# Kernel optimization log

Hardware: AMD Instinct MI355X
Metric: run time of the kernel (lower is better)

Reference implementation:

```python
import jax, jax.numpy as jnp
import numpy as np
from jax import lax

B, T_SRC, C_IN = 32, 1024, 512
CH, T_DE = 256, 4096
K, K_EMB = 5, 3
LEAKY = 0.3
EPS = 1e-5


def setup_inputs() -> dict:
    key = jax.random.key(0)
    ks = jax.random.split(key, 8)
    s = 0.02
    return {
        "x": jax.random.normal(ks[0], (B, T_SRC, C_IN), jnp.float32),
        "target": jax.random.normal(ks[1], (B, 1, T_DE), jnp.float32),
        "dr": jax.random.randint(ks[2], (B, T_SRC), 0, 4),
        "mask": jnp.zeros((B, T_SRC), bool),
        "w_conv1": jax.random.normal(ks[3], (CH, C_IN, K), jnp.float32) * s,
        "b_conv1": jnp.zeros((CH,), jnp.float32),
        "ln1_g": jnp.ones((CH,), jnp.float32),
        "ln1_b": jnp.zeros((CH,), jnp.float32),
        "w_conv2": jax.random.normal(ks[4], (CH, CH, K), jnp.float32) * s,
        "b_conv2": jnp.zeros((CH,), jnp.float32),
        "ln2_g": jnp.ones((CH,), jnp.float32),
        "ln2_b": jnp.zeros((CH,), jnp.float32),
        "w_lin": jax.random.normal(ks[5], (CH, 1), jnp.float32) * s,
        "b_lin": jnp.zeros((1,), jnp.float32),
        "w_emb": jax.random.normal(ks[6], (CH, 1, K_EMB), jnp.float32) * s,
        "b_emb": jnp.zeros((CH,), jnp.float32),
    }


def _conv1d(x, w, b, pad):
    # x: [B, C_in, T], w: [C_out, C_in, K]
    y = lax.conv_general_dilated(x, w, (1,), [(pad, pad)], dimension_numbers=("NCH", "OIH", "NCH"))
    return y + b[None, :, None]


def _layernorm(x, g, b):
    m = jnp.mean(x, -1, keepdims=True)
    v = jnp.var(x, -1, keepdims=True)
    return (x - m) * lax.rsqrt(v + EPS) * g + b


def _average_over_durations(values, durs):
    # values: [B, 1, T_de], durs: [B, T_en] -> [B, 1, T_en]
    ends = jnp.cumsum(durs, 1)                                   # [B, T_en]
    starts = jnp.pad(ends[:, :-1], ((0, 0), (1, 0)))
    nz_cum = jnp.pad(jnp.cumsum((values != 0.0).astype(jnp.float32), 2), ((0, 0), (0, 0), (1, 0)))
    v_cum = jnp.pad(jnp.cumsum(values, 2), ((0, 0), (0, 0), (1, 0)))
    dce = ends[:, None, :]
    dcs = starts[:, None, :]
    sums = jnp.take_along_axis(v_cum, dce, 2) - jnp.take_along_axis(v_cum, dcs, 2)
    nel = jnp.take_along_axis(nz_cum, dce, 2) - jnp.take_along_axis(nz_cum, dcs, 2)
    return jnp.where(nel == 0.0, 0.0, sums / nel)


def reference(x, target, dr, mask, w_conv1, b_conv1, ln1_g, ln1_b, w_conv2, b_conv2, ln2_g, ln2_b, w_lin, b_lin, w_emb, b_emb):
    # VariancePredictor: [conv -> leaky_relu -> layernorm] x2 -> linear -> mask (eval mode, dropout off)
    h = _conv1d(x.transpose(0, 2, 1), w_conv1, b_conv1, (K - 1) // 2).transpose(0, 2, 1)
    h = _layernorm(jax.nn.leaky_relu(h, LEAKY), ln1_g, ln1_b)
    h = _conv1d(h.transpose(0, 2, 1), w_conv2, b_conv2, (K - 1) // 2).transpose(0, 2, 1)
    h = _layernorm(jax.nn.leaky_relu(h, LEAKY), ln2_g, ln2_b)
    energy_pred = (h @ w_lin + b_lin)[..., 0]                     # [B, T_src]
    energy_pred = jnp.where(mask, 0.0, energy_pred)
    avg_energy_target = _average_over_durations(target, dr)       # [B, 1, T_src]
    energy_emb = _conv1d(avg_energy_target, w_emb, b_emb, (K_EMB - 1) // 2)  # [B, CH, T_src]
    return energy_pred, avg_energy_target, energy_emb
```

## Files before the change

### kernel.cpp

```cpp
#include <hip/hip_runtime.h>

typedef __attribute__((ext_vector_type(8))) short short8;
typedef __attribute__((ext_vector_type(4))) float f32x4;

#define LEAKY_F 0.3f

typedef __attribute__((address_space(3))) void lds_t;
typedef __attribute__((address_space(1))) void gmem_t;
#define G2L(g, l) __builtin_amdgcn_global_load_lds((const gmem_t*)(g), (lds_t*)(l), 16, 0, 0)

__device__ __forceinline__ unsigned short f2bf(float f) {
    union { float f; unsigned u; } v; v.f = f;
    unsigned u = v.u;
    return (unsigned short)((u + 0x7fffu + ((u >> 16) & 1u)) >> 16);
}
__device__ __forceinline__ float bf2f(unsigned short u) {
    union { unsigned u; float f; } v; v.u = ((unsigned)u) << 16; return v.f;
}

__global__ void cast_pad_x(const float* __restrict__ in, unsigned short* __restrict__ out) {
    int i = blockIdx.x * 256 + threadIdx.x;
    long g = (long)i * 8;
    int row = (int)(g >> 9);
    int b = row >> 10;
    long o = ((long)(row + (b << 2) + 2) << 9) + (g & 511);
    const float4* p = (const float4*)(in + g);
    float4 a = p[0], c = p[1];
    union { unsigned short s[8]; uint4 v; } u;
    u.s[0] = f2bf(a.x); u.s[1] = f2bf(a.y); u.s[2] = f2bf(a.z); u.s[3] = f2bf(a.w);
    u.s[4] = f2bf(c.x); u.s[5] = f2bf(c.y); u.s[6] = f2bf(c.z); u.s[7] = f2bf(c.w);
    *(uint4*)(out + o) = u.v;
}

__global__ void zero_pads(unsigned short* __restrict__ p, int cin) {
    int j = blockIdx.x * 256 + threadIdx.x;
    int upb = cin >> 1;
    int b = j / upb, rem = j % upb;
    int upr = cin >> 3;
    int r4 = rem / upr;
    int col = (rem % upr) * 8;
    int rowp = (r4 < 2) ? r4 : (r4 + 1024);
    *(uint4*)(p + ((long)b * 1028 + rowp) * cin + col) = make_uint4(0u, 0u, 0u, 0u);
}

__global__ void prep_w(const float* __restrict__ w, unsigned short* __restrict__ out, int CIN, int n) {
    int i = blockIdx.x * 256 + threadIdx.x;
    if (i >= n) return;
    int ch = i / (CIN * 5);
    int rem = i % (CIN * 5);
    int tap = rem / CIN;
    int cin = rem % CIN;
    out[ch * (5 * CIN) + tap * CIN + cin] = f2bf(w[(ch * CIN + cin) * 5 + tap]);
}

template<int CIN, bool PRED>
__global__ __launch_bounds__(512, 1) void gemm_conv_fused(
    const unsigned short* __restrict__ A,
    const unsigned short* __restrict__ W,
    const float* __restrict__ bias,
    const float* __restrict__ gam,
    const float* __restrict__ bet,
    const float* __restrict__ wlin,
    const float* __restrict__ blin,
    const unsigned char* __restrict__ mask,
    unsigned short* __restrict__ Yln,
    float* __restrict__ Ypred)
{
    constexpr int KW = 5 * CIN;
    constexpr int S  = KW / 64;
    constexpr int ASLOT = 128 * 64;
    constexpr int BSLOT = 256 * 64;
    __shared__ __align__(16) unsigned short smem[3 * (ASLOT + BSLOT)];

    const int tid = threadIdx.x, lane = tid & 63, wid = tid >> 6;
    const int wm = wid >> 2, wn = wid & 3;
    const int blk = blockIdx.x;
    const int bb = blk >> 3, tl0 = (blk & 7) << 7;
    const long rowbase = (long)bb * 1028 + tl0;

    long asrc[2]; int adst[2];
    #pragma unroll
    for (int c = 0; c < 2; c++) {
        int u = ((c * 8 + wid) << 6) + lane;
        int r = u >> 3, sg = (u & 7) ^ (r & 7);
        asrc[c] = (rowbase + r) * (long)CIN + sg * 8;
        adst[c] = (c * 8 + wid) << 9;
    }
    long bsrc[4]; int bdst[4];
    #pragma unroll
    for (int c = 0; c < 4; c++) {
        int u = ((c * 8 + wid) << 6) + lane;
        int r = u >> 3, sg = (u & 7) ^ (r & 7);
        bsrc[c] = (long)r * KW + sg * 8;
        bdst[c] = (c * 8 + wid) << 9;
    }

    f32x4 acc[4][4] = {};

    auto stage = [&](int t, int slot) {
        const int k0 = t * 64;
        unsigned short* a = smem + slot * ASLOT;
        unsigned short* b = smem + 3 * ASLOT + slot * BSLOT;
        #pragma unroll
        for (int c = 0; c < 2; c++) G2L(A + asrc[c] + k0, a + adst[c]);
        #pragma unroll
        for (int c = 0; c < 4; c++) G2L(W + bsrc[c] + k0, b + bdst[c]);
    };

    const int l15 = lane & 15, lhi = (lane >> 4) & 3;
    const int arow = (wm * 64 + l15) * 64;
    const int brow = (wn * 64 + l15) * 64;
    const int sw = l15 & 7;

    auto compute = [&](int slot) {
        const unsigned short* ab = smem + slot * ASLOT;
        const unsigned short* bp = smem + 3 * ASLOT + slot * BSLOT;
        #pragma unroll
        for (int kh = 0; kh < 2; kh++) {
            short8 af[4], bg[4];
            const int sgoff = (((kh << 2) | lhi) ^ sw) << 3;
            #pragma unroll
            for (int m = 0; m < 4; m++)
                af[m] = *(const short8*)&ab[arow + m * 1024 + sgoff];
            #pragma unroll
            for (int n = 0; n < 4; n++)
                bg[n] = *(const short8*)&bp[brow + n * 1024 + sgoff];
            asm volatile("s_waitcnt lgkmcnt(0)" ::: "memory");
            __builtin_amdgcn_sched_barrier(0);
            __builtin_amdgcn_s_setprio(1);
            #pragma unroll
            for (int m = 0; m < 4; m++)
                #pragma unroll
                for (int n = 0; n < 4; n++)
                    acc[m][n] = __builtin_amdgcn_mfma_f32_16x16x32_bf16(af[m], bg[n], acc[m][n], 0, 0, 0);
            __builtin_amdgcn_s_setprio(0);
            __builtin_amdgcn_sched_barrier(0);
            if (kh == 0) __builtin_amdgcn_s_barrier();
        }
    };

    stage(0, 0);
    stage(1, 1);

    int rb = 0;
    #pragma unroll 1
    for (int t = 0; t < S - 2; ++t) {
        asm volatile("s_waitcnt vmcnt(6)" ::: "memory");
        __builtin_amdgcn_sched_barrier(0);
        __builtin_amdgcn_s_barrier();
        __builtin_amdgcn_sched_barrier(0);
        stage(t + 2, (rb == 0) ? 2 : (rb - 1));
        compute(rb);
        rb = (rb == 2) ? 0 : (rb + 1);
    }
    asm volatile("s_waitcnt vmcnt(6)" ::: "memory");
    __builtin_amdgcn_sched_barrier(0);
    __builtin_amdgcn_s_barrier();
    __builtin_amdgcn_sched_barrier(0);
    compute(rb);
    rb = (rb == 2) ? 0 : (rb + 1);
    asm volatile("s_waitcnt vmcnt(0)" ::: "memory");
    __builtin_amdgcn_sched_barrier(0);
    __builtin_amdgcn_s_barrier();
    __builtin_amdgcn_sched_barrier(0);
    compute(rb);

    __syncthreads();

    float* pb = (float*)((char*)smem + 65536);
    if (tid < 256) {
        pb[tid]       = bias[tid];
        pb[256 + tid] = gam[tid];
        pb[512 + tid] = bet[tid];
        pb[768 + tid] = PRED ? wlin[tid] : 0.f;
    }
    __syncthreads();

    unsigned short* tile = smem;
    #pragma unroll
    for (int n = 0; n < 4; n++) {
        const int col = wn * 64 + n * 16 + l15;
        const float bv = pb[col];
        const int u0 = col >> 3, ce = col & 7;
        #pragma unroll
        for (int m = 0; m < 4; m++) {
            const int rA = wm * 64 + m * 16 + lhi * 4;
            #pragma unroll
            for (int q = 0; q < 4; q++) {
                const int row = rA + q;
                float v = acc[m][n][q] + bv;
                v = v > 0.f ? v : LEAKY_F * v;
                tile[row * 256 + ((u0 ^ (row & 7)) << 3) + ce] = f2bf(v);
            }
        }
    }
    __syncthreads();

    const int rid = tid >> 2, jq = tid & 3;
    const int r7 = rid & 7;
    float vals[8][8];
    float s1 = 0.f, s2 = 0.f, sgw = 0.f, sgc = 0.f, sbw = 0.f;
    #pragma unroll
    for (int u4 = 0; u4 < 8; u4++) {
        const int u = u4 * 4 + jq;
        short8 pk = *(const short8*)&tile[rid * 256 + ((u ^ r7) << 3)];
        #pragma unroll
        for (int e = 0; e < 8; e++) {
            float v = bf2f((unsigned short)pk[e]);
            vals[u4][e] = v;
            s1 += v; s2 += v * v;
        }
        if (PRED) {
            const int c0 = u * 8;
            f32x4 ga = *(const f32x4*)&pb[256 + c0], gb = *(const f32x4*)&pb[260 + c0];
            f32x4 wa = *(const f32x4*)&pb[768 + c0], wb = *(const f32x4*)&pb[772 + c0];
            f32x4 ba = *(const f32x4*)&pb[512 + c0], bb2 = *(const f32x4*)&pb[516 + c0];
            #pragma unroll
            for (int e = 0; e < 4; e++) {
                sgw += vals[u4][e] * ga[e] * wa[e] + vals[u4][e + 4] * gb[e] * wb[e];
                sgc += ga[e] * wa[e] + gb[e] * wb[e];
                sbw += ba[e] * wa[e] + bb2[e] * wb[e];
            }
        }
    }
    s1 += __shfl_xor(s1, 1); s1 += __shfl_xor(s1, 2);
    s2 += __shfl_xor(s2, 1); s2 += __shfl_xor(s2, 2);
    const float mean = s1 * (1.f / 256.f);
    const float var  = s2 * (1.f / 256.f) - mean * mean;
    const float rs   = rsqrtf(var + 1e-5f);
    const long grow  = (long)blk * 128 + rid;

    if (PRED) {
        sgw += __shfl_xor(sgw, 1); sgw += __shfl_xor(sgw, 2);
        sgc += __shfl_xor(sgc, 1); sgc += __shfl_xor(sgc, 2);
        sbw += __shfl_xor(sbw, 1); sbw += __shfl_xor(sbw, 2);
        if (jq == 0) {
            float p = rs * (sgw - mean * sgc) + sbw + blin[0];
            if (mask[grow]) p = 0.f;
            Ypred[grow] = p;
        }
    } else {
        const int bnum = (int)(grow >> 10);
        const long prow = grow + (bnum << 2) + 2;
        #pragma unroll
        for (int u4 = 0; u4 < 8; u4++) {
            const int u = u4 * 4 + jq;
            const int c0 = u * 8;
            f32x4 ga = *(const f32x4*)&pb[256 + c0], gb = *(const f32x4*)&pb[260 + c0];
            f32x4 ba = *(const f32x4*)&pb[512 + c0], bb2 = *(const f32x4*)&pb[516 + c0];
            union { unsigned short s[8]; uint4 v; } o;
            #pragma unroll
            for (int e = 0; e < 4; e++) {
                o.s[e]     = f2bf((vals[u4][e]     - mean) * rs * ga[e] + ba[e]);
                o.s[e + 4] = f2bf((vals[u4][e + 4] - mean) * rs * gb[e] + bb2[e]);
            }
            *(uint4*)(Yln + prow * 256 + c0) = o.v;
        }
    }
}

__global__ void avg_kernel(const float* __restrict__ target, const int* __restrict__ dr,
                           float* __restrict__ outAvg) {
    __shared__ float vcum[4097];
    __shared__ float ncum[4097];
    __shared__ float sS[256];
    __shared__ float sC[256];
    __shared__ int   sI[256];
    int b = blockIdx.x, tid = threadIdx.x;
    const float* tb = target + b * 4096;
    float lv[16]; float ls = 0.f, lc = 0.f;
    #pragma unroll
    for (int j = 0; j < 16; j++) {
        float v = tb[tid * 16 + j]; lv[j] = v; ls += v; lc += (v != 0.f) ? 1.f : 0.f;
    }
    sS[tid] = ls; sC[tid] = lc;
    __syncthreads();
    for (int off = 1; off < 256; off <<= 1) {
        float a = 0.f, c2 = 0.f;
        if (tid >= off) { a = sS[tid - off]; c2 = sC[tid - off]; }
        __syncthreads();
        sS[tid] += a; sC[tid] += c2;
        __syncthreads();
    }
    float pS = tid ? sS[tid - 1] : 0.f, pC = tid ? sC[tid - 1] : 0.f;
    if (tid == 0) { vcum[0] = 0.f; ncum[0] = 0.f; }
    float run = pS, runc = pC;
    #pragma unroll
    for (int j = 0; j < 16; j++) {
        run += lv[j]; runc += (lv[j] != 0.f) ? 1.f : 0.f;
        vcum[tid * 16 + j + 1] = run; ncum[tid * 16 + j + 1] = runc;
    }
    const int* db = dr + b * 1024;
    int ld[4]; int lsum = 0;
    #pragma unroll
    for (int j = 0; j < 4; j++) { ld[j] = db[tid * 4 + j]; lsum += ld[j]; }
    sI[tid] = lsum;
    __syncthreads();
    for (int off = 1; off < 256; off <<= 1) {
        int a = 0; if (tid >= off) a = sI[tid - off];
        __syncthreads();
        sI[tid] += a;
        __syncthreads();
    }
    int run2 = tid ? sI[tid - 1] : 0;
    #pragma unroll
    for (int j = 0; j < 4; j++) {
        run2 += ld[j];
        int e = run2, s0 = e - ld[j];
        float sums = vcum[e] - vcum[s0];
        float cnt  = ncum[e] - ncum[s0];
        outAvg[b * 1024 + tid * 4 + j] = (cnt == 0.f) ? 0.f : sums / cnt;
    }
}

__global__ void emb_kernel(const float* __restrict__ avg, const float* __restrict__ wemb,
                           const float* __restrict__ bemb, float* __restrict__ out) {
    int id = blockIdx.x * 256 + threadIdx.x;
    int t4 = id & 255;
    int ch = (id >> 8) & 255;
    int b  = id >> 16;
    int t0 = t4 * 4;
    const float* a = avg + b * 1024;
    float am1 = (t0 - 1 >= 0) ? a[t0 - 1] : 0.f;
    float a0 = a[t0], a1 = a[t0 + 1], a2 = a[t0 + 2], a3 = a[t0 + 3];
    float a4 = (t0 + 4 < 1024) ? a[t0 + 4] : 0.f;
    float w0 = wemb[ch * 3], w1 = wemb[ch * 3 + 1], w2 = wemb[ch * 3 + 2], bb = bemb[ch];
    float4 o;
    o.x = bb + am1 * w0 + a0 * w1 + a1 * w2;
    o.y = bb + a0 * w0 + a1 * w1 + a2 * w2;
    o.z = bb + a1 * w0 + a2 * w1 + a3 * w2;
    o.w = bb + a2 * w0 + a3 * w1 + a4 * w2;
    *(float4*)(out + (((b << 8) | ch) << 10) + t0) = o;
}

extern "C" void kernel_launch(void* const* d_in, const int* in_sizes, int n_in,
                              void* d_out, int out_size, void* d_ws, size_t ws_size,
                              hipStream_t stream) {
    const float* x      = (const float*)d_in[0];
    const float* target = (const float*)d_in[1];
    const int*   dr     = (const int*)d_in[2];
    const unsigned char* mask = (const unsigned char*)d_in[3];
    const float* w1   = (const float*)d_in[4];
    const float* b1   = (const float*)d_in[5];
    const float* g1   = (const float*)d_in[6];
    const float* be1  = (const float*)d_in[7];
    const float* w2   = (const float*)d_in[8];
    const float* b2   = (const float*)d_in[9];
    const float* g2   = (const float*)d_in[10];
    const float* be2  = (const float*)d_in[11];
    const float* wlin = (const float*)d_in[12];
    const float* blin = (const float*)d_in[13];
    const float* wemb = (const float*)d_in[14];
    const float* bemb = (const float*)d_in[15];

    char* ws = (char*)d_ws;
    unsigned short* xbp  = (unsigned short*)ws;
    unsigned short* h1bp = (unsigned short*)(ws + 33685504);
    unsigned short* wr1  = (unsigned short*)(ws + 50528256);
    unsigned short* wr2  = (unsigned short*)(ws + 51838976);

    float* outPred = (float*)d_out;
    float* outAvg  = outPred + 32768;
    float* outEmb  = outPred + 65536;

    cast_pad_x<<<8192, 256, 0, stream>>>(x, xbp);
    zero_pads<<<32, 256, 0, stream>>>(xbp, 512);
    zero_pads<<<16, 256, 0, stream>>>(h1bp, 256);
    prep_w<<<2560, 256, 0, stream>>>(w1, wr1, 512, 256 * 512 * 5);
    prep_w<<<1280, 256, 0, stream>>>(w2, wr2, 256, 256 * 256 * 5);
    gemm_conv_fused<512, false><<<256, 512, 0, stream>>>(
        xbp, wr1, b1, g1, be1, wlin, blin, mask, h1bp, outPred);
    gemm_conv_fused<256, true><<<256, 512, 0, stream>>>(
        h1bp, wr2, b2, g2, be2, wlin, blin, mask, h1bp, outPred);
    avg_kernel<<<32, 256, 0, stream>>>(target, dr, outAvg);
    emb_kernel<<<8192, 256, 0, stream>>>(outAvg, wemb, bemb, outEmb);
}
```

Baseline: 121.0 us.

## Enlarge conv GEMM tile to 256x256 with double-buffered phased pipeline

The fused conv GEMM now computes 256 time rows per block instead of 128, so each block reuses the 256-channel weight tile across twice as many rows and halves total weight traffic. The K-loop changes from a three-slot ring to a double buffer split into four phases, each issuing part of the next tile's global-to-LDS loads while doing MFMAs on two 16-row groups. The LayerNorm epilogue loops over two 128-row halves. The grid drops from 256 to 128 blocks, which leaves many of the MI355X's compute units idle, and the doubled accumulator count raises register pressure.

```diff
diff --git a/kernel.cpp b/kernel.cpp
--- a/kernel.cpp
+++ b/kernel.cpp
@@ -68,106 +68,106 @@
 {
     constexpr int KW = 5 * CIN;
     constexpr int S  = KW / 64;
-    constexpr int ASLOT = 128 * 64;
-    constexpr int BSLOT = 256 * 64;
-    __shared__ __align__(16) unsigned short smem[3 * (ASLOT + BSLOT)];
+    __shared__ __align__(16) unsigned short smem[65536];
+    __shared__ float pb[1024];
 
     const int tid = threadIdx.x, lane = tid & 63, wid = tid >> 6;
     const int wm = wid >> 2, wn = wid & 3;
     const int blk = blockIdx.x;
-    const int bb = blk >> 3, tl0 = (blk & 7) << 7;
+    const int bb = blk >> 2, tl0 = (blk & 3) << 8;
     const long rowbase = (long)bb * 1028 + tl0;
 
-    long asrc[2]; int adst[2];
+    long asrc[2], bsrc[2]; int udst[2];
     #pragma unroll
     for (int c = 0; c < 2; c++) {
-        int u = ((c * 8 + wid) << 6) + lane;
+        int u = c * 512 + tid;
         int r = u >> 3, sg = (u & 7) ^ (r & 7);
         asrc[c] = (rowbase + r) * (long)CIN + sg * 8;
-        adst[c] = (c * 8 + wid) << 9;
-    }
-    long bsrc[4]; int bdst[4];
-    #pragma unroll
-    for (int c = 0; c < 4; c++) {
-        int u = ((c * 8 + wid) << 6) + lane;
-        int r = u >> 3, sg = (u & 7) ^ (r & 7);
         bsrc[c] = (long)r * KW + sg * 8;
-        bdst[c] = (c * 8 + wid) << 9;
-    }
-
-    f32x4 acc[4][4] = {};
-
-    auto stage = [&](int t, int slot) {
-        const int k0 = t * 64;
-        unsigned short* a = smem + slot * ASLOT;
-        unsigned short* b = smem + 3 * ASLOT + slot * BSLOT;
+        udst[c] = u * 8;
+    }
+
+    auto stageA = [&](int buf, int h, int kt) {
+        const long k0 = (long)kt * 64 + (long)h * 128 * CIN;
         #pragma unroll
-        for (int c = 0; c < 2; c++) G2L(A + asrc[c] + k0, a + adst[c]);
+        for (int c = 0; c < 2; c++)
+            G2L(A + asrc[c] + k0, &smem[buf * 16384 + h * 8192 + udst[c]]);
+    };
+    auto stageB = [&](int buf, int h, int kt) {
+        const long k0 = (long)kt * 64 + (long)h * 128 * KW;
         #pragma unroll
-        for (int c = 0; c < 4; c++) G2L(W + bsrc[c] + k0, b + bdst[c]);
+        for (int c = 0; c < 2; c++)
+            G2L(W + bsrc[c] + k0, &smem[32768 + buf * 16384 + h * 8192 + udst[c]]);
     };
 
-    const int l15 = lane & 15, lhi = (lane >> 4) & 3;
-    const int arow = (wm * 64 + l15) * 64;
-    const int brow = (wn * 64 + l15) * 64;
-    const int sw = l15 & 7;
-
-    auto compute = [&](int slot) {
-        const unsigned short* ab = smem + slot * ASLOT;
-        const unsigned short* bp = smem + 3 * ASLOT + slot * BSLOT;
-        #pragma unroll
-        for (int kh = 0; kh < 2; kh++) {
-            short8 af[4], bg[4];
-            const int sgoff = (((kh << 2) | lhi) ^ sw) << 3;
-            #pragma unroll
-            for (int m = 0; m < 4; m++)
-                af[m] = *(const short8*)&ab[arow + m * 1024 + sgoff];
-            #pragma unroll
-            for (int n = 0; n < 4; n++)
-                bg[n] = *(const short8*)&bp[brow + n * 1024 + sgoff];
-            asm volatile("s_waitcnt lgkmcnt(0)" ::: "memory");
-            __builtin_amdgcn_sched_barrier(0);
-            __builtin_amdgcn_s_setprio(1);
-            #pragma unroll
-            for (int m = 0; m < 4; m++)
-                #pragma unroll
-                for (int n = 0; n < 4; n++)
-                    acc[m][n] = __builtin_amdgcn_mfma_f32_16x16x32_bf16(af[m], bg[n], acc[m][n], 0, 0, 0);
-            __builtin_amdgcn_s_setprio(0);
-            __builtin_amdgcn_sched_barrier(0);
-            if (kh == 0) __builtin_amdgcn_s_barrier();
-        }
-    };
-
-    stage(0, 0);
-    stage(1, 1);
-
-    int rb = 0;
+    const int l15 = lane & 15, lhi = (lane >> 4) & 3, sw = l15 & 7;
+    const int arow0 = wm * 128 + l15;
+    const int brow0 = wn * 64 + l15;
+
+    f32x4 acc[8][4] = {};
+    short8 bg[4][2];
+
+#define READ_B(buf)                                                             \
+    _Pragma("unroll")                                                           \
+    for (int n = 0; n < 4; n++)                                                 \
+        _Pragma("unroll")                                                       \
+        for (int kh = 0; kh < 2; kh++)                                          \
+            bg[n][kh] = *(const short8*)&smem[32768 + (buf) * 16384 +           \
+                (brow0 + n * 16) * 64 + ((((kh << 2) | lhi) ^ sw) << 3)];
+
+#define PHASE(buf, mp, STAGE, VMW)                                              \
+    {                                                                           \
+        short8 af[2][2];                                                        \
+        _Pragma("unroll")                                                       \
+        for (int j = 0; j < 2; j++)                                             \
+            _Pragma("unroll")                                                   \
+            for (int kh = 0; kh < 2; kh++)                                      \
+                af[j][kh] = *(const short8*)&smem[(buf) * 16384 +               \
+                    (arow0 + ((mp) * 2 + j) * 16) * 64 + ((((kh << 2) | lhi) ^ sw) << 3)]; \
+        STAGE;                                                                  \
+        VMW;                                                                    \
+        __builtin_amdgcn_s_barrier();                                           \
+        asm volatile("s_waitcnt lgkmcnt(0)" ::: "memory");                      \
+        __builtin_amdgcn_sched_barrier(0);                                      \
+        __builtin_amdgcn_s_setprio(1);                                          \
+        _Pragma("unroll")                                                       \
+        for (int j = 0; j < 2; j++)                                             \
+            _Pragma("unroll")                                                   \
+            for (int n = 0; n < 4; n++)                                         \
+                _Pragma("unroll")                                               \
+                for (int kh = 0; kh < 2; kh++)                                  \
+                    acc[(mp) * 2 + j][n] = __builtin_amdgcn_mfma_f32_16x16x32_bf16( \
+                        af[j][kh], bg[n][kh], acc[(mp) * 2 + j][n], 0, 0, 0);   \
+        __builtin_amdgcn_s_setprio(0);                                          \
+        __builtin_amdgcn_sched_barrier(0);                                      \
+        __builtin_amdgcn_s_barrier();                                           \
+    }
+
+    stageB(0, 0, 0); stageB(0, 1, 0); stageA(0, 0, 0); stageA(0, 1, 0);
+    asm volatile("s_waitcnt vmcnt(2)" ::: "memory");
+    __builtin_amdgcn_s_barrier();
+
     #pragma unroll 1
-    for (int t = 0; t < S - 2; ++t) {
-        asm volatile("s_waitcnt vmcnt(6)" ::: "memory");
-        __builtin_amdgcn_sched_barrier(0);
-        __builtin_amdgcn_s_barrier();
-        __builtin_amdgcn_sched_barrier(0);
-        stage(t + 2, (rb == 0) ? 2 : (rb - 1));
-        compute(rb);
-        rb = (rb == 2) ? 0 : (rb + 1);
-    }
-    asm volatile("s_waitcnt vmcnt(6)" ::: "memory");
-    __builtin_amdgcn_sched_barrier(0);
-    __builtin_amdgcn_s_barrier();
-    __builtin_amdgcn_sched_barrier(0);
-    compute(rb);
-    rb = (rb == 2) ? 0 : (rb + 1);
-    asm volatile("s_waitcnt vmcnt(0)" ::: "memory");
-    __builtin_amdgcn_sched_barrier(0);
-    __builtin_amdgcn_s_barrier();
-    __builtin_amdgcn_sched_barrier(0);
-    compute(rb);
-
-    __syncthreads();
-
-    float* pb = (float*)((char*)smem + 65536);
+    for (int t = 0; t < S - 1; ++t) {
+        const int b = t & 1, nb = b ^ 1;
+        READ_B(b);
+        PHASE(b, 0, stageB(nb, 0, t + 1), );
+        PHASE(b, 1, stageB(nb, 1, t + 1), asm volatile("s_waitcnt vmcnt(4)" ::: "memory"));
+        PHASE(b, 2, stageA(nb, 0, t + 1), );
+        PHASE(b, 3, stageA(nb, 1, t + 1), asm volatile("s_waitcnt vmcnt(2)" ::: "memory"));
+    }
+    {
+        const int b = (S - 1) & 1;
+        READ_B(b);
+        PHASE(b, 0, , );
+        PHASE(b, 1, , asm volatile("s_waitcnt vmcnt(0)" ::: "memory"));
+        PHASE(b, 2, , );
+        PHASE(b, 3, , );
+    }
+#undef PHASE
+#undef READ_B
+
+    __syncthreads();
     if (tid < 256) {
         pb[tid]       = bias[tid];
         pb[256 + tid] = gam[tid];
@@ -176,85 +176,87 @@
     }
     __syncthreads();
 
-    unsigned short* tile = smem;
-    #pragma unroll
-    for (int n = 0; n < 4; n++) {
-        const int col = wn * 64 + n * 16 + l15;
-        const float bv = pb[col];
-        const int u0 = col >> 3, ce = col & 7;
+    #pragma unroll
+    for (int mm = 0; mm < 8; mm++) {
         #pragma unroll
-        for (int m = 0; m < 4; m++) {
-            const int rA = wm * 64 + m * 16 + lhi * 4;
+        for (int n = 0; n < 4; n++) {
+            const int col = wn * 64 + n * 16 + l15;
+            const int u0 = col >> 3, ce = col & 7;
+            const float bv = pb[col];
             #pragma unroll
             for (int q = 0; q < 4; q++) {
-                const int row = rA + q;
-                float v = acc[m][n][q] + bv;
+                const int row = wm * 128 + mm * 16 + lhi * 4 + q;
+                float v = acc[mm][n][q] + bv;
                 v = v > 0.f ? v : LEAKY_F * v;
-                tile[row * 256 + ((u0 ^ (row & 7)) << 3) + ce] = f2bf(v);
+                smem[row * 256 + ((u0 ^ (row & 7)) << 3) + ce] = f2bf(v);
             }
         }
     }
     __syncthreads();
 
     const int rid = tid >> 2, jq = tid & 3;
-    const int r7 = rid & 7;
-    float vals[8][8];
-    float s1 = 0.f, s2 = 0.f, sgw = 0.f, sgc = 0.f, sbw = 0.f;
-    #pragma unroll
-    for (int u4 = 0; u4 < 8; u4++) {
-        const int u = u4 * 4 + jq;
-        short8 pk = *(const short8*)&tile[rid * 256 + ((u ^ r7) << 3)];
-        #pragma unroll
-        for (int e = 0; e < 8; e++) {
-            float v = bf2f((unsigned short)pk[e]);
-            vals[u4][e] = v;
-            s1 += v; s2 += v * v;
-        }
-        if (PRED) {
-            const int c0 = u * 8;
-            f32x4 ga = *(const f32x4*)&pb[256 + c0], gb = *(const f32x4*)&pb[260 + c0];
-            f32x4 wa = *(const f32x4*)&pb[768 + c0], wb = *(const f32x4*)&pb[772 + c0];
-            f32x4 ba = *(const f32x4*)&pb[512 + c0], bb2 = *(const f32x4*)&pb[516 + c0];
-            #pragma unroll
-            for (int e = 0; e < 4; e++) {
-                sgw += vals[u4][e] * ga[e] * wa[e] + vals[u4][e + 4] * gb[e] * wb[e];
-                sgc += ga[e] * wa[e] + gb[e] * wb[e];
-                sbw += ba[e] * wa[e] + bb2[e] * wb[e];
-            }
-        }
-    }
-    s1 += __shfl_xor(s1, 1); s1 += __shfl_xor(s1, 2);
-    s2 += __shfl_xor(s2, 1); s2 += __shfl_xor(s2, 2);
-    const float mean = s1 * (1.f / 256.f);
-    const float var  = s2 * (1.f / 256.f) - mean * mean;
-    const float rs   = rsqrtf(var + 1e-5f);
-    const long grow  = (long)blk * 128 + rid;
-
-    if (PRED) {
-        sgw += __shfl_xor(sgw, 1); sgw += __shfl_xor(sgw, 2);
-        sgc += __shfl_xor(sgc, 1); sgc += __shfl_xor(sgc, 2);
-        sbw += __shfl_xor(sbw, 1); sbw += __shfl_xor(sbw, 2);
-        if (jq == 0) {
-            float p = rs * (sgw - mean * sgc) + sbw + blin[0];
-            if (mask[grow]) p = 0.f;
-            Ypred[grow] = p;
-        }
-    } else {
-        const int bnum = (int)(grow >> 10);
-        const long prow = grow + (bnum << 2) + 2;
+    #pragma unroll 1
+    for (int ro = 0; ro < 2; ro++) {
+        const int row = ro * 128 + rid;
+        const int r7 = row & 7;
+        float vals[8][8];
+        float s1 = 0.f, s2 = 0.f, sgw = 0.f, sgc = 0.f, sbw = 0.f;
         #pragma unroll
         for (int u4 = 0; u4 < 8; u4++) {
             const int u = u4 * 4 + jq;
-            const int c0 = u * 8;
-            f32x4 ga = *(const f32x4*)&pb[256 + c0], gb = *(const f32x4*)&pb[260 + c0];
-            f32x4 ba = *(const f32x4*)&pb[512 + c0], bb2 = *(const f32x4*)&pb[516 + c0];
-            union { unsigned short s[8]; uint4 v; } o;
+            short8 pk = *(const short8*)&smem[row * 256 + ((u ^ r7) << 3)];
             #pragma unroll
-            for (int e = 0; e < 4; e++) {
-                o.s[e]     = f2bf((vals[u4][e]     - mean) * rs * ga[e] + ba[e]);
-                o.s[e + 4] = f2bf((vals[u4][e + 4] - mean) * rs * gb[e] + bb2[e]);
-            }
-            *(uint4*)(Yln + prow * 256 + c0) = o.v;
+            for (int e = 0; e < 8; e++) {
+                float v = bf2f((unsigned short)pk[e]);
+                vals[u4][e] = v;
+                s1 += v; s2 += v * v;
+            }
+            if (PRED) {
+                const int c0 = u * 8;
+                f32x4 ga = *(const f32x4*)&pb[256 + c0], gb = *(const f32x4*)&pb[260 + c0];
+                f32x4 wa = *(const f32x4*)&pb[768 + c0], wb = *(const f32x4*)&pb[772 + c0];
+                f32x4 ba = *(const f32x4*)&pb[512 + c0], bb2 = *(const f32x4*)&pb[516 + c0];
+                #pragma unroll
+                for (int e = 0; e < 4; e++) {
+                    sgw += vals[u4][e] * ga[e] * wa[e] + vals[u4][e + 4] * gb[e] * wb[e];
+                    sgc += ga[e] * wa[e] + gb[e] * wb[e];
+                    sbw += ba[e] * wa[e] + bb2[e] * wb[e];
+                }
+            }
+        }
+        s1 += __shfl_xor(s1, 1); s1 += __shfl_xor(s1, 2);
+        s2 += __shfl_xor(s2, 1); s2 += __shfl_xor(s2, 2);
+        const float mean = s1 * (1.f / 256.f);
+        const float var  = s2 * (1.f / 256.f) - mean * mean;
+        const float rs   = rsqrtf(var + 1e-5f);
+        const long grow  = (long)blk * 256 + row;
+
+        if (PRED) {
+            sgw += __shfl_xor(sgw, 1); sgw += __shfl_xor(sgw, 2);
+            sgc += __shfl_xor(sgc, 1); sgc += __shfl_xor(sgc, 2);
+            sbw += __shfl_xor(sbw, 1); sbw += __shfl_xor(sbw, 2);
+            if (jq == 0) {
+                float p = rs * (sgw - mean * sgc) + sbw + blin[0];
+                if (mask[grow]) p = 0.f;
+                Ypred[grow] = p;
+            }
+        } else {
+            const int bnum = (int)(grow >> 10);
+            const long prow = grow + (bnum << 2) + 2;
+            #pragma unroll
+            for (int u4 = 0; u4 < 8; u4++) {
+                const int u = u4 * 4 + jq;
+                const int c0 = u * 8;
+                f32x4 ga = *(const f32x4*)&pb[256 + c0], gb = *(const f32x4*)&pb[260 + c0];
+                f32x4 ba = *(const f32x4*)&pb[512 + c0], bb2 = *(const f32x4*)&pb[516 + c0];
+                union { unsigned short s[8]; uint4 v; } o;
+                #pragma unroll
+                for (int e = 0; e < 4; e++) {
+                    o.s[e]     = f2bf((vals[u4][e]     - mean) * rs * ga[e] + ba[e]);
+                    o.s[e + 4] = f2bf((vals[u4][e + 4] - mean) * rs * gb[e] + bb2[e]);
+                }
+                *(uint4*)(Yln + prow * 256 + c0) = o.v;
+            }
         }
     }
 }
@@ -368,9 +370,9 @@
     zero_pads<<<16, 256, 0, stream>>>(h1bp, 256);
     prep_w<<<2560, 256, 0, stream>>>(w1, wr1, 512, 256 * 512 * 5);
     prep_w<<<1280, 256, 0, stream>>>(w2, wr2, 256, 256 * 256 * 5);
-    gemm_conv_fused<512, false><<<256, 512, 0, stream>>>(
+    gemm_conv_fused<512, false><<<128, 512, 0, stream>>>(
         xbp, wr1, b1, g1, be1, wlin, blin, mask, h1bp, outPred);
-    gemm_conv_fused<256, true><<<256, 512, 0, stream>>>(
+    gemm_conv_fused<256, true><<<128, 512, 0, stream>>>(
         h1bp, wr2, b2, g2, be2, wlin, blin, mask, h1bp, outPred);
     avg_kernel<<<32, 256, 0, stream>>>(target, dr, outAvg);
     emb_kernel<<<8192, 256, 0, stream>>>(outAvg, wemb, bemb, outEmb);
```

After: 167.6 us. 1.39x slower.

## Restructure the conv GEMM main loop with early LDS fragment loads and a single barrier

Applied to the files above, without the earlier changes.

Inlines the compute step into the main loop. Both k-halves of the A/B fragments are read from LDS up front, and the next global-to-LDS stage is issued between those reads, so the mid-iteration barrier can be dropped. The separate tail iterations are folded into the loop with a conditional vmcnt wait, and the epilogue parameter buffer gets its own shared array. Launch bounds change to 512 threads with 2 blocks per CU, which caps the register budget; the shared-memory footprint likely still allows only one block, so this mainly risks register spills, since more fragments are now held live at once.

```diff
diff --git a/kernel.cpp b/kernel.cpp
--- a/kernel.cpp
+++ b/kernel.cpp
@@ -54,7 +54,7 @@
 }
 
 template<int CIN, bool PRED>
-__global__ __launch_bounds__(512, 1) void gemm_conv_fused(
+__global__ __launch_bounds__(512, 2) void gemm_conv_fused(
     const unsigned short* __restrict__ A,
     const unsigned short* __restrict__ W,
     const float* __restrict__ bias,
@@ -71,6 +71,7 @@
     constexpr int ASLOT = 128 * 64;
     constexpr int BSLOT = 256 * 64;
     __shared__ __align__(16) unsigned short smem[3 * (ASLOT + BSLOT)];
+    __shared__ float pb[1024];
 
     const int tid = threadIdx.x, lane = tid & 63, wid = tid >> 6;
     const int wm = wid >> 2, wn = wid & 3;
@@ -95,8 +96,6 @@
         bdst[c] = (c * 8 + wid) << 9;
     }
 
-    f32x4 acc[4][4] = {};
-
     auto stage = [&](int t, int slot) {
         const int k0 = t * 64;
         unsigned short* a = smem + slot * ASLOT;
@@ -107,67 +106,73 @@
         for (int c = 0; c < 4; c++) G2L(W + bsrc[c] + k0, b + bdst[c]);
     };
 
-    const int l15 = lane & 15, lhi = (lane >> 4) & 3;
+    const int l15 = lane & 15, lhi = (lane >> 4) & 3, sw = l15 & 7;
     const int arow = (wm * 64 + l15) * 64;
     const int brow = (wn * 64 + l15) * 64;
-    const int sw = l15 & 7;
-
-    auto compute = [&](int slot) {
-        const unsigned short* ab = smem + slot * ASLOT;
-        const unsigned short* bp = smem + 3 * ASLOT + slot * BSLOT;
-        #pragma unroll
-        for (int kh = 0; kh < 2; kh++) {
-            short8 af[4], bg[4];
-            const int sgoff = (((kh << 2) | lhi) ^ sw) << 3;
-            #pragma unroll
-            for (int m = 0; m < 4; m++)
-                af[m] = *(const short8*)&ab[arow + m * 1024 + sgoff];
-            #pragma unroll
-            for (int n = 0; n < 4; n++)
-                bg[n] = *(const short8*)&bp[brow + n * 1024 + sgoff];
-            asm volatile("s_waitcnt lgkmcnt(0)" ::: "memory");
-            __builtin_amdgcn_sched_barrier(0);
-            __builtin_amdgcn_s_setprio(1);
-            #pragma unroll
-            for (int m = 0; m < 4; m++)
-                #pragma unroll
-                for (int n = 0; n < 4; n++)
-                    acc[m][n] = __builtin_amdgcn_mfma_f32_16x16x32_bf16(af[m], bg[n], acc[m][n], 0, 0, 0);
-            __builtin_amdgcn_s_setprio(0);
-            __builtin_amdgcn_sched_barrier(0);
-            if (kh == 0) __builtin_amdgcn_s_barrier();
-        }
-    };
+    const int sg0 = ((lhi ^ sw) & 7) << 3;
+    const int sg1 = (((4 | lhi) ^ sw) & 7) << 3;
+
+    f32x4 acc[4][4] = {};
 
     stage(0, 0);
     stage(1, 1);
 
     int rb = 0;
     #pragma unroll 1
-    for (int t = 0; t < S - 2; ++t) {
-        asm volatile("s_waitcnt vmcnt(6)" ::: "memory");
+    for (int t = 0; t < S; ++t) {
+        if (t < S - 1) { asm volatile("s_waitcnt vmcnt(6)" ::: "memory"); }
+        else           { asm volatile("s_waitcnt vmcnt(0)" ::: "memory"); }
         __builtin_amdgcn_sched_barrier(0);
         __builtin_amdgcn_s_barrier();
         __builtin_amdgcn_sched_barrier(0);
-        stage(t + 2, (rb == 0) ? 2 : (rb - 1));
-        compute(rb);
+
+        const unsigned short* ab = smem + rb * ASLOT;
+        const unsigned short* bp = smem + 3 * ASLOT + rb * BSLOT;
+
+        short8 af0[4], bg0[4], af1[4], bg1[4];
+        #pragma unroll
+        for (int m = 0; m < 4; m++)
+            af0[m] = *(const short8*)&ab[arow + m * 1024 + sg0];
+        #pragma unroll
+        for (int n = 0; n < 4; n++)
+            bg0[n] = *(const short8*)&bp[brow + n * 1024 + sg0];
+
+        if (t + 2 < S) stage(t + 2, (rb == 0) ? 2 : (rb - 1));
+
+        #pragma unroll
+        for (int m = 0; m < 4; m++)
+            af1[m] = *(const short8*)&ab[arow + m * 1024 + sg1];
+        #pragma unroll
+        for (int n = 0; n < 4; n++)
+            bg1[n] = *(const short8*)&bp[brow + n * 1024 + sg1];
+
+        asm volatile("s_waitcnt lgkmcnt(8)" ::: "memory");
+        __builtin_amdgcn_sched_barrier(0);
+        __builtin_amdgcn_s_setprio(1);
+        #pragma unroll
+        for (int m = 0; m < 4; m++)
+            #pragma unroll
+            for (int n = 0; n < 4; n++)
+                acc[m][n] = __builtin_amdgcn_mfma_f32_16x16x32_bf16(af0[m], bg0[n], acc[m][n], 0, 0, 0);
+        __builtin_amdgcn_s_setprio(0);
+        __builtin_amdgcn_sched_barrier(0);
+
+        asm volatile("s_waitcnt lgkmcnt(0)" ::: "memory");
+        __builtin_amdgcn_sched_barrier(0);
+        __builtin_amdgcn_s_setprio(1);
+        #pragma unroll
+        for (int m = 0; m < 4; m++)
+            #pragma unroll
+            for (int n = 0; n < 4; n++)
+                acc[m][n] = __builtin_amdgcn_mfma_f32_16x16x32_bf16(af1[m], bg1[n], acc[m][n], 0, 0, 0);
+        __builtin_amdgcn_s_setprio(0);
+        __builtin_amdgcn_sched_barrier(0);
+
         rb = (rb == 2) ? 0 : (rb + 1);
     }
-    asm volatile("s_waitcnt vmcnt(6)" ::: "memory");
-    __builtin_amdgcn_sched_barrier(0);
-    __builtin_amdgcn_s_barrier();
-    __builtin_amdgcn_sched_barrier(0);
-    compute(rb);
-    rb = (rb == 2) ? 0 : (rb + 1);
-    asm volatile("s_waitcnt vmcnt(0)" ::: "memory");
-    __builtin_amdgcn_sched_barrier(0);
-    __builtin_amdgcn_s_barrier();
-    __builtin_amdgcn_sched_barrier(0);
-    compute(rb);
-
-    __syncthreads();
-
-    float* pb = (float*)((char*)smem + 65536);
+
+    __syncthreads();
+
     if (tid < 256) {
         pb[tid]       = bias[tid];
         pb[256 + tid] = gam[tid];
```

Result: slower. 135.7 us (+12.1%).
